# Kernel tuning notes

Hardware: AMD Instinct MI355X
Metric: run time of the kernel (lower is better)

Reference implementation:

```python
import jax, jax.numpy as jnp
import numpy as np

N, E, L, HID, HEADS, G = 50000, 800000, 2, 128, 8, 256
DK = HID // HEADS

def _ln(x, g, b, eps=1e-5):
    m = jnp.mean(x, axis=-1, keepdims=True)
    v = jnp.mean((x - m) ** 2, axis=-1, keepdims=True)
    return (x - m) * jax.lax.rsqrt(v + eps) * g + b

def setup_inputs() -> dict:
    key = jax.random.key(0)
    ks = jax.random.split(key, 24)
    rn = lambda i, s: (0.05 * jax.random.normal(ks[i], s)).astype(jnp.float32)
    return {
        'node_attr': jax.random.randint(ks[0], (N, 4), 0, 64, dtype=jnp.int32),
        'batch_idx': jnp.sort(jax.random.randint(ks[1], (N,), 0, G, dtype=jnp.int32)),
        'edge_index': jax.random.randint(ks[2], (2, E), 0, N, dtype=jnp.int32),
        'strat_dist': jax.random.randint(ks[3], (E,), 0, 32, dtype=jnp.int32),
        'strat_path': jax.random.randint(ks[4], (E,), 0, 16, dtype=jnp.int32),
        'atom_emb': rn(5, (4, 64, HID)),
        'dist_emb': rn(6, (L, 32, HID)),
        'path_emb': rn(7, (L, 16, HID)),
        'Wq': rn(8, (L, HID, HID)), 'bq': rn(9, (L, HID)),
        'Wk': rn(10, (L, HID, HID)), 'bk': rn(11, (L, HID)),
        'Wv': rn(12, (L, HID, HID)), 'bv': rn(13, (L, HID)),
        'Wa': rn(14, (L, HID, HID)), 'ba': rn(15, (L, HID)),
        'ln1_g': jnp.ones((L, HID), jnp.float32), 'ln1_b': jnp.zeros((L, HID), jnp.float32),
        'Wmid': rn(16, (L, HID, 2 * HID)), 'bmid': rn(17, (L, 2 * HID)),
        'Wo': rn(18, (L, 2 * HID, HID)), 'bo': rn(19, (L, HID)),
        'ln2_g': jnp.ones((L, HID), jnp.float32), 'ln2_b': jnp.zeros((L, HID), jnp.float32),
        'W_out': rn(20, (HID, 1)), 'b_out': jnp.zeros((1,), jnp.float32),
    }

def reference(node_attr, batch_idx, edge_index, strat_dist, strat_path,
              atom_emb, dist_emb, path_emb, Wq, bq, Wk, bk, Wv, bv, Wa, ba,
              ln1_g, ln1_b, Wmid, bmid, Wo, bo, ln2_g, ln2_b, W_out, b_out):
    # node encoder: sum of per-feature embeddings (AtomEncoder style)
    x = sum(atom_emb[f][node_attr[:, f]] for f in range(node_attr.shape[1]))  # [N, HID]
    src, tgt = edge_index[0], edge_index[1]  # j (source), i (target)
    inv_sqrt_dk = np.float32(1.0 / np.sqrt(DK))
    for l in range(L):
        # per-edge gather + relational encodings added to the source vector
        s = x[src] + dist_emb[l][strat_dist] + path_emb[l][strat_path]  # [E, HID]
        t = x[tgt]                                                      # [E, HID]
        q = (t @ Wq[l] + bq[l]).reshape(E, HEADS, DK)
        k = (s @ Wk[l] + bk[l]).reshape(E, HEADS, DK)
        v = (s @ Wv[l] + bv[l]).reshape(E, HEADS, DK)
        scores = jnp.sum(q * k, axis=-1) * inv_sqrt_dk  # [E, HEADS]
        # segment softmax keyed on target node id
        smax = jax.ops.segment_max(scores, tgt, num_segments=N)
        ex = jnp.exp(scores - smax[tgt])
        den = jax.ops.segment_sum(ex, tgt, num_segments=N)
        att = ex / (den[tgt] + 1e-16)                   # [E, HEADS]
        msg = (v * att[:, :, None]).reshape(E, HID)
        aggr = jax.ops.segment_sum(msg, tgt, num_segments=N)  # scatter-add
        # update: attn FFN + residual + LayerNorms (dropout is identity in eval)
        h = _ln(jax.nn.gelu(aggr, approximate=False) @ Wa[l] + ba[l] + x, ln1_g[l], ln1_b[l])
        h2 = jax.nn.gelu(h @ Wmid[l] + bmid[l], approximate=False) @ Wo[l] + bo[l]
        x = _ln(h2 + h, ln2_g[l], ln2_b[l])
    # global mean pool per graph, then readout
    cnt = jax.ops.segment_sum(jnp.ones((N,), x.dtype), batch_idx, num_segments=G)
    pooled = jax.ops.segment_sum(x, batch_idx, num_segments=G) / jnp.maximum(cnt, 1.0)[:, None]
    return pooled @ W_out + b_out
```

## Files before the change

### kernel.cpp

```cpp
#include <hip/hip_runtime.h>
#include <hip/hip_bf16.h>
#include <math.h>
#include <stdint.h>

#define N_NODES 50000
#define N_EDGES 800000
#define HID 128
#define NGRAPH 256
#define NLAYER 2
#define CAP 64

#define SCATH 704
#define EHALF 360448
#define SCATQ 859

#define CPAD 5

#define ENC_B 3125
#define TKV_B (ENC_B + 1024)
#define RPK_B (TKV_B + 128)
#define PREP_B (RPK_B + 4)

typedef __bf16 bf16x8 __attribute__((ext_vector_type(8)));
typedef __bf16 bf16x2 __attribute__((ext_vector_type(2)));
typedef float f32x4 __attribute__((ext_vector_type(4)));
typedef float f32x2 __attribute__((ext_vector_type(2)));

__device__ __forceinline__ float gelu_f(float v) {
    return 0.5f * v * (1.0f + erff(v * 0.70710678118654752f));
}

__device__ __forceinline__ f32x2 f8lo(uint32_t d) {
    return __builtin_amdgcn_cvt_pk_f32_fp8((int)d, false);
}
__device__ __forceinline__ f32x2 f8hi(uint32_t d) {
    return __builtin_amdgcn_cvt_pk_f32_fp8((int)d, true);
}
__device__ __forceinline__ uint32_t pk4_fp8(float a, float b, float c, float d) {
    int w = __builtin_amdgcn_cvt_pk_fp8_f32(a, b, 0, false);
    w = __builtin_amdgcn_cvt_pk_fp8_f32(c, d, w, true);
    return (uint32_t)w;
}
__device__ __forceinline__ f32x2 bfpair(uint32_t d) {
    f32x2 r;
    r[0] = __uint_as_float(d << 16);
    r[1] = __uint_as_float(d);
    return r;
}

__device__ __forceinline__ void scatter_block(
    int blk, int ebase, int elim,
    const int* __restrict__ tgt, const int* __restrict__ src,
    const int* __restrict__ sd, const int* __restrict__ sp,
    int* __restrict__ cnt, uint32_t* __restrict__ ei) {
    int tid = threadIdx.x;
    int e0 = ebase + blk * 512 + tid;
    int e1 = e0 + 256;
    bool v0 = e0 < elim;
    bool v1 = e1 < elim;
    int t0 = 0, t1 = 0;
    uint32_t p0 = 0, p1 = 0;
    if (v0) {
        t0 = tgt[e0];
        p0 = (uint32_t)src[e0] | ((uint32_t)((sd[e0] << 4) | sp[e0]) << 16);
    }
    if (v1) {
        t1 = tgt[e1];
        p1 = (uint32_t)src[e1] | ((uint32_t)((sd[e1] << 4) | sp[e1]) << 16);
    }
    int r0 = CAP, r1 = CAP;
    if (v0) r0 = atomicAdd(&cnt[t0 << CPAD], 1);
    if (v1) r1 = atomicAdd(&cnt[t1 << CPAD], 1);
    if (v0 && r0 < CAP) ei[(t0 << 6) + r0] = p0;
    if (v1 && r1 < CAP) ei[(t1 << 6) + r1] = p1;
}

__global__ __launch_bounds__(256) void prep_kernel(
    const int* __restrict__ attr, const float* __restrict__ aemb,
    __bf16* __restrict__ xb,
    const float* __restrict__ de, const float* __restrict__ pe,
    const float* __restrict__ Wk, const float* __restrict__ Wv,
    __bf16* __restrict__ tkv,
    const float* __restrict__ Wq, const float* __restrict__ Wa,
    const float* __restrict__ Wmid, const float* __restrict__ Wo,
    __bf16* __restrict__ wqkvf, __bf16* __restrict__ waf,
    __bf16* __restrict__ wmidf, __bf16* __restrict__ wof,
    const int* __restrict__ batch, const float* __restrict__ bout,
    const float* __restrict__ bq, const float* __restrict__ bk,
    const float* __restrict__ bv,
    float* __restrict__ invc, float* __restrict__ outp, float* __restrict__ bqkv,
    const int* __restrict__ tgt, const int* __restrict__ src,
    const int* __restrict__ sd, const int* __restrict__ sp,
    int* __restrict__ cnt, uint32_t* __restrict__ ei) {
    __shared__ float sde[128];
    int b = blockIdx.x;
    int tid = threadIdx.x;
    if (b < SCATH) {
        scatter_block(b, 0, EHALF, tgt, src, sd, sp, cnt, ei);
        return;
    }
    b -= SCATH;
    if (b < ENC_B) {
        int gid = b * 256 + tid;
        int n = gid >> 4;
        int c8 = (gid & 15) << 3;
        const int4 a = *(const int4*)(attr + n * 4);
        const float* r0 = aemb + (size_t)(0 * 64 + a.x) * 128 + c8;
        const float* r1 = aemb + (size_t)(1 * 64 + a.y) * 128 + c8;
        const float* r2 = aemb + (size_t)(2 * 64 + a.z) * 128 + c8;
        const float* r3 = aemb + (size_t)(3 * 64 + a.w) * 128 + c8;
        f32x4 v0a = *(const f32x4*)r0, v0b = *(const f32x4*)(r0 + 4);
        f32x4 v1a = *(const f32x4*)r1, v1b = *(const f32x4*)(r1 + 4);
        f32x4 v2a = *(const f32x4*)r2, v2b = *(const f32x4*)(r2 + 4);
        f32x4 v3a = *(const f32x4*)r3, v3b = *(const f32x4*)(r3 + 4);
        bf16x8 o;
#pragma unroll
        for (int j = 0; j < 4; j++) {
            o[j] = (__bf16)(v0a[j] + v1a[j] + v2a[j] + v3a[j]);
            o[4 + j] = (__bf16)(v0b[j] + v1b[j] + v2b[j] + v3b[j]);
        }
        *(bf16x8*)(xb + (size_t)n * 128 + c8) = o;
    } else if (b < TKV_B) {
        int bb = b - ENC_B;
        int l = bb >> 9;
        int md = bb & 511;
        int dd = md >> 4, pp = md & 15;
        int c = tid;
        if (c < 128) sde[c] = de[l * 4096 + dd * 128 + c] + pe[l * 2048 + pp * 128 + c];
        __syncthreads();
        const float* W = (c < 128) ? (Wk + l * 16384) : (Wv + l * 16384);
        int cc = c & 127;
        float acc = 0.f;
#pragma unroll 4
        for (int k = 0; k < 128; k++) acc = fmaf(sde[k], W[k * 128 + cc], acc);
        tkv[(size_t)bb * 256 + c] = (__bf16)acc;
    } else if (b < RPK_B) {
        int u = (b - TKV_B) * 256 + tid;
        int l = u >> 14, r = u & 16383;
        const float* srcp;
        __bf16* dstp;
        int kg, scol, srcCO;
        if (r < 6144) {
            kg = r / 384;
            int uu = r % 384;
            int sec = uu >> 7, cc = uu & 127;
            scol = ((cc & 15) << 3) | (cc >> 4);
            const float* Ws = (sec == 0) ? Wq : (sec == 1) ? Wk : Wv;
            srcp = Ws + l * 16384;
            srcCO = 128;
            dstp = wqkvf + (size_t)l * 49152 + (size_t)r * 8;
        } else if (r < 8192) {
            int rr = r - 6144;
            kg = rr >> 7;
            int cc = rr & 127;
            scol = ((cc & 15) << 3) | (cc >> 4);
            srcp = Wa + l * 16384;
            srcCO = 128;
            dstp = waf + (size_t)l * 16384 + (size_t)rr * 8;
        } else if (r < 12288) {
            int rr = r - 8192;
            kg = rr >> 8;
            int uu = rr & 255;
            int blk = uu >> 7, cc = uu & 127;
            scol = blk * 128 + (((cc & 15) << 3) | (cc >> 4));
            srcp = Wmid + l * 32768;
            srcCO = 256;
            dstp = wmidf + (size_t)l * 32768 + (size_t)rr * 8;
        } else {
            int rr = r - 12288;
            kg = rr >> 7;
            int cc = rr & 127;
            scol = ((cc & 15) << 3) | (cc >> 4);
            srcp = Wo + l * 32768;
            srcCO = 128;
            dstp = wof + (size_t)l * 32768 + (size_t)rr * 8;
        }
        bf16x8 o;
#pragma unroll
        for (int j = 0; j < 8; j++) o[j] = (__bf16)srcp[(kg * 8 + j) * srcCO + scol];
        *(bf16x8*)dstp = o;
    } else {
        int sb = b - RPK_B;
        if (sb == 0) {
            int g = tid;
            int lo = 0, hi = N_NODES;
            while (lo < hi) { int mid = (lo + hi) >> 1; if (batch[mid] < g) lo = mid + 1; else hi = mid; }
            int start = lo;
            lo = start; hi = N_NODES;
            while (lo < hi) { int mid = (lo + hi) >> 1; if (batch[mid] < g + 1) lo = mid + 1; else hi = mid; }
            int c2 = lo - start;
            invc[g] = 1.0f / fmaxf((float)c2, 1.0f);
            outp[g] = bout[0];
        } else {
            int r = (sb - 1) * 256 + tid;
            int l = r / 384, c = r % 384;
            float v = (c < 128) ? bq[l * 128 + c]
                    : (c < 256) ? bk[l * 128 + c - 128]
                                : bv[l * 128 + c - 256];
            bqkv[r] = v;
        }
    }
}

__global__ __launch_bounds__(256) void qkv_gemm(
    const __bf16* __restrict__ A, const __bf16* __restrict__ Wf,
    const float* __restrict__ bias, __bf16* __restrict__ Qb,
    uint8_t* __restrict__ kv8, int M, int scatN,
    const int* __restrict__ tgt, const int* __restrict__ src,
    const int* __restrict__ sd, const int* __restrict__ sp,
    int* __restrict__ cnt, uint32_t* __restrict__ ei) {
    int tid = threadIdx.x;
    if (blockIdx.x < (unsigned)scatN) {
        scatter_block(blockIdx.x, EHALF, N_EDGES, tgt, src, sd, sp, cnt, ei);
        return;
    }
    int bq = blockIdx.x - scatN;
    int sec = bq % 3;
    int rowblk = bq / 3;
    int lane = tid & 63;
    int wv = tid >> 6;
    int row0 = rowblk * 64 + wv * 16;
    int col0 = sec * 128;
    if (row0 >= M) return;
    int quad = lane >> 4, tq = lane & 15;
    f32x4 acc[8] = {};
#pragma unroll
    for (int k0 = 0; k0 < 128; k0 += 32) {
        int rr = row0 + tq;
        if (rr >= M) rr = M - 1;
        bf16x8 af = *(const bf16x8*)(A + (size_t)rr * 128 + k0 + quad * 8);
#pragma unroll
        for (int nt = 0; nt < 8; nt++) {
            bf16x8 bfr = *(const bf16x8*)(Wf + ((size_t)((k0 >> 3) + quad) * 384 + col0 + nt * 16 + tq) * 8);
            acc[nt] = __builtin_amdgcn_mfma_f32_16x16x32_bf16(af, bfr, acc[nt], 0, 0, 0);
        }
    }
    int cb = tq * 8;
    float bia[8];
#pragma unroll
    for (int t = 0; t < 8; t++) bia[t] = bias[col0 + cb + t];
#pragma unroll
    for (int v = 0; v < 4; v++) {
        int rr = row0 + quad * 4 + v;
        if (rr >= M) continue;
        float val[8];
#pragma unroll
        for (int t = 0; t < 8; t++) val[t] = acc[t][v] + bia[t];
        if (sec == 0) {
            bf16x8 ov;
#pragma unroll
            for (int t = 0; t < 8; t++) ov[t] = (__bf16)val[t];
            *(bf16x8*)(Qb + (size_t)rr * 128 + cb) = ov;
        } else {
            uint2 st;
            st.x = pk4_fp8(val[0], val[1], val[2], val[3]);
            st.y = pk4_fp8(val[4], val[5], val[6], val[7]);
            *(uint2*)(kv8 + (size_t)rr * 256 + (sec - 1) * 128 + cb) = st;
        }
    }
}

template <bool POOL>
__global__ __launch_bounds__(256) void ffn_uber(
    const __bf16* __restrict__ A,
    const __bf16* __restrict__ xres,
    const __bf16* __restrict__ Waf, const float* __restrict__ ba,
    const float* __restrict__ l1g, const float* __restrict__ l1b,
    const __bf16* __restrict__ Wmf, const float* __restrict__ bmid,
    const __bf16* __restrict__ Wof, const float* __restrict__ bo,
    const float* __restrict__ l2g, const float* __restrict__ l2b,
    __bf16* __restrict__ outx,
    const int* __restrict__ batch, const float* __restrict__ invc,
    const float* __restrict__ WoutV, float* __restrict__ outp,
    int M) {
    __shared__ __bf16 hld[4][16][136];
    __shared__ __bf16 smid[4][16][264];
    __shared__ float ps[POOL ? NGRAPH : 1];
    int lane = threadIdx.x & 63;
    int wv = threadIdx.x >> 6;
    int row0 = blockIdx.x * 64 + wv * 16;
    bool active = row0 < M;
    if (POOL) {
        ps[threadIdx.x] = 0.f;
        __syncthreads();
    } else if (!active) {
        return;
    }
    int quad = lane >> 4, tq = lane & 15;
    if (active) {
        int cb = tq * 8;
        {
            f32x4 acc[8] = {};
#pragma unroll
            for (int k0 = 0; k0 < 128; k0 += 32) {
                int rr = row0 + tq;
                if (rr >= M) rr = M - 1;
                bf16x8 af = *(const bf16x8*)(A + (size_t)rr * 128 + k0 + quad * 8);
#pragma unroll
                for (int nt = 0; nt < 8; nt++) {
                    bf16x8 bfr = *(const bf16x8*)(Waf + ((size_t)((k0 >> 3) + quad) * 128 + nt * 16 + tq) * 8);
                    acc[nt] = __builtin_amdgcn_mfma_f32_16x16x32_bf16(af, bfr, acc[nt], 0, 0, 0);
                }
            }
            float bia[8], gv[8], bv2[8];
#pragma unroll
            for (int t = 0; t < 8; t++) {
                bia[t] = ba[cb + t];
                gv[t] = l1g[cb + t];
                bv2[t] = l1b[cb + t];
            }
#pragma unroll
            for (int v = 0; v < 4; v++) {
                int rr = row0 + quad * 4 + v;
                int rc = (rr < M) ? rr : M - 1;
                bf16x8 rv = *(const bf16x8*)(xres + (size_t)rc * 128 + cb);
                float val[8];
#pragma unroll
                for (int t = 0; t < 8; t++) val[t] = acc[t][v] + bia[t] + (float)rv[t];
                float s = 0.f, s2 = 0.f;
#pragma unroll
                for (int t = 0; t < 8; t++) { s += val[t]; s2 = fmaf(val[t], val[t], s2); }
#pragma unroll
                for (int o = 1; o < 16; o <<= 1) {
                    s += __shfl_xor(s, o);
                    s2 += __shfl_xor(s2, o);
                }
                float m = s * (1.0f / 128.0f);
                float var = s2 * (1.0f / 128.0f) - m * m;
                float rs = rsqrtf(var + 1e-5f);
                bf16x8 ov;
#pragma unroll
                for (int t = 0; t < 8; t++) ov[t] = (__bf16)((val[t] - m) * rs * gv[t] + bv2[t]);
                *(bf16x8*)(&hld[wv][quad * 4 + v][cb]) = ov;
            }
        }
        asm volatile("" ::: "memory");
#pragma unroll
        for (int cH = 0; cH < 2; ++cH) {
            f32x4 acc[8] = {};
#pragma unroll
            for (int k0 = 0; k0 < 128; k0 += 32) {
                bf16x8 af = *(const bf16x8*)(&hld[wv][tq][k0 + quad * 8]);
#pragma unroll
                for (int nt = 0; nt < 8; nt++) {
                    bf16x8 bfr = *(const bf16x8*)(Wmf + ((size_t)((k0 >> 3) + quad) * 256 + cH * 128 + nt * 16 + tq) * 8);
                    acc[nt] = __builtin_amdgcn_mfma_f32_16x16x32_bf16(af, bfr, acc[nt], 0, 0, 0);
                }
            }
            int cb2 = cH * 128 + cb;
            float bia[8];
#pragma unroll
            for (int t = 0; t < 8; t++) bia[t] = bmid[cb2 + t];
#pragma unroll
            for (int v = 0; v < 4; v++) {
                bf16x8 ov;
#pragma unroll
                for (int t = 0; t < 8; t++) ov[t] = (__bf16)gelu_f(acc[t][v] + bia[t]);
                *(bf16x8*)(&smid[wv][quad * 4 + v][cb2]) = ov;
            }
        }
        asm volatile("" ::: "memory");
        f32x4 acc[8] = {};
#pragma unroll
        for (int k0 = 0; k0 < 256; k0 += 32) {
            bf16x8 af = *(const bf16x8*)(&smid[wv][tq][k0 + quad * 8]);
#pragma unroll
            for (int nt = 0; nt < 8; nt++) {
                bf16x8 bfr = *(const bf16x8*)(Wof + ((size_t)((k0 >> 3) + quad) * 128 + nt * 16 + tq) * 8);
                acc[nt] = __builtin_amdgcn_mfma_f32_16x16x32_bf16(af, bfr, acc[nt], 0, 0, 0);
            }
        }
        float bia[8], gv[8], bv2[8], wo8[8];
#pragma unroll
        for (int t = 0; t < 8; t++) {
            bia[t] = bo[cb + t];
            gv[t] = l2g[cb + t];
            bv2[t] = l2b[cb + t];
        }
        if (POOL) {
#pragma unroll
            for (int t = 0; t < 8; t++) wo8[t] = WoutV[cb + t];
        }
#pragma unroll
        for (int v = 0; v < 4; v++) {
            int rr = row0 + quad * 4 + v;
            bf16x8 rv = *(const bf16x8*)(&hld[wv][quad * 4 + v][cb]);
            float val[8];
#pragma unroll
            for (int t = 0; t < 8; t++) val[t] = acc[t][v] + bia[t] + (float)rv[t];
            float s = 0.f, s2 = 0.f;
#pragma unroll
            for (int t = 0; t < 8; t++) { s += val[t]; s2 = fmaf(val[t], val[t], s2); }
#pragma unroll
            for (int o = 1; o < 16; o <<= 1) {
                s += __shfl_xor(s, o);
                s2 += __shfl_xor(s2, o);
            }
            float m = s * (1.0f / 128.0f);
            float var = s2 * (1.0f / 128.0f) - m * m;
            float rs = rsqrtf(var + 1e-5f);
#pragma unroll
            for (int t = 0; t < 8; t++) val[t] = (val[t] - m) * rs * gv[t] + bv2[t];
            if (rr >= M) continue;
            if (!POOL) {
                bf16x8 ov;
#pragma unroll
                for (int t = 0; t < 8; t++) ov[t] = (__bf16)val[t];
                *(bf16x8*)(outx + (size_t)rr * 128 + cb) = ov;
            } else {
                float dot = 0.f;
#pragma unroll
                for (int t = 0; t < 8; t++) dot = fmaf(val[t], wo8[t], dot);
#pragma unroll
                for (int o = 1; o < 16; o <<= 1) dot += __shfl_xor(dot, o);
                if (tq == 0) {
                    int g = batch[rr];
                    atomicAdd(&ps[g], dot * invc[g]);
                }
            }
        }
    }
    if (POOL) {
        __syncthreads();
        float pv = ps[threadIdx.x];
        if (pv != 0.f) atomicAdd(&outp[threadIdx.x], pv);
    }
}

__global__ __launch_bounds__(256) void attn_kernel(
    const __bf16* __restrict__ Qb, const uint8_t* __restrict__ kv8,
    const __bf16* __restrict__ tkv,
    const int* __restrict__ cnt, const uint32_t* __restrict__ ei,
    __bf16* __restrict__ outb) {
    __shared__ float red[4][1376];
    int wv = threadIdx.x >> 6;
    int i = blockIdx.x * 4 + wv;
    int lane = threadIdx.x & 63;
    int slot = lane >> 3, h = lane & 7;
    int ch0 = h * 16;
    const uint4* qv = (const uint4*)(Qb + (size_t)i * 128 + ch0);
    uint4 qa = qv[0], qb = qv[1];
    uint32_t qd[8] = {qa.x, qa.y, qa.z, qa.w, qb.x, qb.y, qb.z, qb.w};
    f32x2 qp[8];
#pragma unroll
    for (int j = 0; j < 8; j++) qp[j] = bfpair(qd[j]);
    int deg = cnt[i << CPAD];
    if (deg > CAP) deg = CAP;
    int p0 = i << 6;
    int p1 = p0 + deg;
    float l = 0.f;
    f32x2 ap[8] = {};
    int p = p0 + slot;
    uint32_t w1 = 0, w2 = 0;
    if (p < p1) w1 = ei[p];
    if (p + 8 < p1) w2 = ei[p + 8];
    uint4 kw, vw, t0, t1, u0, u1;
    {
        int j = w1 & 0xffff, md = w1 >> 16;
        const uint8_t* kr = kv8 + (size_t)j * 256 + ch0;
        kw = *(const uint4*)kr;
        vw = *(const uint4*)(kr + 128);
        const __bf16* tr = tkv + md * 256 + ch0;
        t0 = *(const uint4*)tr;
        t1 = *(const uint4*)(tr + 8);
        u0 = *(const uint4*)(tr + 128);
        u1 = *(const uint4*)(tr + 136);
    }
    while (p < p1) {
        uint4 kwn, vwn, t0n, t1n, u0n, u1n;
        {
            int j = w2 & 0xffff, md = w2 >> 16;
            const uint8_t* kr = kv8 + (size_t)j * 256 + ch0;
            kwn = *(const uint4*)kr;
            vwn = *(const uint4*)(kr + 128);
            const __bf16* tr = tkv + md * 256 + ch0;
            t0n = *(const uint4*)tr;
            t1n = *(const uint4*)(tr + 8);
            u0n = *(const uint4*)(tr + 128);
            u1n = *(const uint4*)(tr + 136);
        }
        int pn = p + 16;
        uint32_t w3 = ei[(pn < p1) ? pn : p];
        uint32_t kd[4] = {kw.x, kw.y, kw.z, kw.w};
        uint32_t vd[4] = {vw.x, vw.y, vw.z, vw.w};
        uint32_t td[8] = {t0.x, t0.y, t0.z, t0.w, t1.x, t1.y, t1.z, t1.w};
        uint32_t ud[8] = {u0.x, u0.y, u0.z, u0.w, u1.x, u1.y, u1.z, u1.w};
        f32x2 sa = {0.f, 0.f};
#pragma unroll
        for (int j = 0; j < 4; j++) {
            f32x2 klo = f8lo(kd[j]) + bfpair(td[2 * j]);
            f32x2 khi = f8hi(kd[j]) + bfpair(td[2 * j + 1]);
            sa = qp[2 * j] * klo + sa;
            sa = qp[2 * j + 1] * khi + sa;
        }
        float s = sa[0] + sa[1];
        float pe = __expf(s * 0.25f);
        l += pe;
        f32x2 pp = {pe, pe};
#pragma unroll
        for (int j = 0; j < 4; j++) {
            f32x2 vlo = f8lo(vd[j]) + bfpair(ud[2 * j]);
            f32x2 vhi = f8hi(vd[j]) + bfpair(ud[2 * j + 1]);
            ap[2 * j] = pp * vlo + ap[2 * j];
            ap[2 * j + 1] = pp * vhi + ap[2 * j + 1];
        }
        kw = kwn; vw = vwn; t0 = t0n; t1 = t1n; u0 = u0n; u1 = u1n;
        w2 = w3;
        p += 8;
    }
    float* rw = red[wv] + slot * 172 + 20 * h;
#pragma unroll
    for (int j = 0; j < 8; j++) *(f32x2*)(rw + 2 * j) = ap[j];
    red[wv][slot * 172 + 156 + h] = l;
    asm volatile("" ::: "memory");
    int pc = 2 * lane + 4 * (lane >> 3);
    int hh = lane >> 3;
    float s0 = 0.f, s1 = 0.f, ls = 0.f;
#pragma unroll
    for (int s = 0; s < 8; s++) {
        float2 v = *(const float2*)(red[wv] + s * 172 + pc);
        s0 += v.x;
        s1 += v.y;
        ls += red[wv][s * 172 + 156 + hh];
    }
    float inv = 1.0f / (ls + 1e-16f);
    bf16x2 o2;
    o2[0] = (__bf16)gelu_f(s0 * inv);
    o2[1] = (__bf16)gelu_f(s1 * inv);
    *(bf16x2*)(outb + (size_t)i * 128 + 2 * lane) = o2;
}

extern "C" void kernel_launch(void* const* d_in, const int* in_sizes, int n_in,
                              void* d_out, int out_size, void* d_ws, size_t ws_size,
                              hipStream_t stream) {
    const int N = N_NODES, E = N_EDGES;
    const int* node_attr = (const int*)d_in[0];
    const int* batch_idx = (const int*)d_in[1];
    const int* edge_index = (const int*)d_in[2];
    const int* strat_dist = (const int*)d_in[3];
    const int* strat_path = (const int*)d_in[4];
    const float* atom_emb = (const float*)d_in[5];
    const float* dist_emb = (const float*)d_in[6];
    const float* path_emb = (const float*)d_in[7];
    const float* Wq = (const float*)d_in[8];
    const float* bq = (const float*)d_in[9];
    const float* Wk = (const float*)d_in[10];
    const float* bk = (const float*)d_in[11];
    const float* Wv = (const float*)d_in[12];
    const float* bv = (const float*)d_in[13];
    const float* Wa = (const float*)d_in[14];
    const float* ba = (const float*)d_in[15];
    const float* ln1g = (const float*)d_in[16];
    const float* ln1b = (const float*)d_in[17];
    const float* Wmid = (const float*)d_in[18];
    const float* bmid = (const float*)d_in[19];
    const float* Wo = (const float*)d_in[20];
    const float* bo = (const float*)d_in[21];
    const float* ln2g = (const float*)d_in[22];
    const float* ln2b = (const float*)d_in[23];
    const float* Wout = (const float*)d_in[24];
    const float* bout = (const float*)d_in[25];
    float* out = (float*)d_out;

    const int* src = edge_index;
    const int* tgt = edge_index + E;

    size_t NF = (size_t)N * HID;
    float* invc = (float*)d_ws;
    float* bqkv = invc + 256;
    __bf16* xb = (__bf16*)(bqkv + 768);
    __bf16* Qb = xb + NF;
    __bf16* ab = Qb + NF;
    __bf16* tkv = ab + NF;
    __bf16* wqkvf = tkv + 262144;
    __bf16* waf = wqkvf + 98304;
    __bf16* wmidf = waf + 32768;
    __bf16* wof = wmidf + 65536;
    uint8_t* kv8 = (uint8_t*)(wof + 65536);
    uint32_t* ei = (uint32_t*)(kv8 + (size_t)N * 256);
    int* cnt = (int*)(ei + (size_t)N * CAP);

    hipMemsetAsync(cnt, 0, (size_t)N * 32 * sizeof(int), stream);
    prep_kernel<<<SCATH + PREP_B, 256, 0, stream>>>(
        node_attr, atom_emb, xb,
        dist_emb, path_emb, Wk, Wv, tkv,
        Wq, Wa, Wmid, Wo, wqkvf, waf, wmidf, wof,
        batch_idx, bout, bq, bk, bv, invc, out, bqkv,
        tgt, src, strat_dist, strat_path, cnt, ei);

    const int GB = (N + 63) / 64;
    const int AB = (N + 3) / 4;

    for (int l = 0; l < NLAYER; ++l) {
        int scatN = (l == 0) ? SCATQ : 0;
        qkv_gemm<<<scatN + 3 * GB, 256, 0, stream>>>(
            xb, wqkvf + l * 49152, bqkv + l * 384, Qb, kv8, N, scatN,
            tgt, src, strat_dist, strat_path, cnt, ei);

        attn_kernel<<<AB, 256, 0, stream>>>(Qb, kv8, tkv + l * 131072, cnt, ei, ab);

        if (l < NLAYER - 1) {
            ffn_uber<false><<<GB, 256, 0, stream>>>(
                ab, xb, waf + l * 16384, ba + l * 128, ln1g + l * 128, ln1b + l * 128,
                wmidf + l * 32768, bmid + l * 256, wof + l * 32768, bo + l * 128,
                ln2g + l * 128, ln2b + l * 128, xb,
                nullptr, nullptr, nullptr, nullptr, N);
        } else {
            ffn_uber<true><<<GB, 256, 0, stream>>>(
                ab, xb, waf + l * 16384, ba + l * 128, ln1g + l * 128, ln1b + l * 128,
                wmidf + l * 32768, bmid + l * 256, wof + l * 32768, bo + l * 128,
                ln2g + l * 128, ln2b + l * 128, nullptr,
                batch_idx, invc, Wout, out, N);
        }
    }
}
```

Before: 371.0 us.

## Move all edge bucketing into prep kernel with target-range partitioned scatter

The edge scatter into per-target buckets no longer runs split across the prep kernel and the first QKV GEMM. It now runs entirely in the prep kernel. Each group of 4096 edges is handled by 8 blocks, and each block only inserts edges whose target falls in its 6250-node range, which localizes atomics and bucket writes. The trade-off is that every block reads tgt for all 4096 edges in its group, so target reads are multiplied 8x. The QKV GEMM also loses its overlap with half of the scatter work.

After: 370.1 us. Within noise of the previous version (-0.3%).

```diff
diff --git a/kernel.cpp b/kernel.cpp
--- a/kernel.cpp
+++ b/kernel.cpp
@@ -10,11 +10,11 @@
 #define NLAYER 2
 #define CAP 64
 
-#define SCATH 704
-#define EHALF 360448
-#define SCATQ 859
-
 #define CPAD 5
+
+#define SC_GRP 196
+#define SC_B (SC_GRP * 8)
+#define NPART 6250
 
 #define ENC_B 3125
 #define TKV_B (ENC_B + 1024)
@@ -46,33 +46,6 @@
     r[0] = __uint_as_float(d << 16);
     r[1] = __uint_as_float(d);
     return r;
-}
-
-__device__ __forceinline__ void scatter_block(
-    int blk, int ebase, int elim,
-    const int* __restrict__ tgt, const int* __restrict__ src,
-    const int* __restrict__ sd, const int* __restrict__ sp,
-    int* __restrict__ cnt, uint32_t* __restrict__ ei) {
-    int tid = threadIdx.x;
-    int e0 = ebase + blk * 512 + tid;
-    int e1 = e0 + 256;
-    bool v0 = e0 < elim;
-    bool v1 = e1 < elim;
-    int t0 = 0, t1 = 0;
-    uint32_t p0 = 0, p1 = 0;
-    if (v0) {
-        t0 = tgt[e0];
-        p0 = (uint32_t)src[e0] | ((uint32_t)((sd[e0] << 4) | sp[e0]) << 16);
-    }
-    if (v1) {
-        t1 = tgt[e1];
-        p1 = (uint32_t)src[e1] | ((uint32_t)((sd[e1] << 4) | sp[e1]) << 16);
-    }
-    int r0 = CAP, r1 = CAP;
-    if (v0) r0 = atomicAdd(&cnt[t0 << CPAD], 1);
-    if (v1) r1 = atomicAdd(&cnt[t1 << CPAD], 1);
-    if (v0 && r0 < CAP) ei[(t0 << 6) + r0] = p0;
-    if (v1 && r1 < CAP) ei[(t1 << 6) + r1] = p1;
 }
 
 __global__ __launch_bounds__(256) void prep_kernel(
@@ -95,11 +68,27 @@
     __shared__ float sde[128];
     int b = blockIdx.x;
     int tid = threadIdx.x;
-    if (b < SCATH) {
-        scatter_block(b, 0, EHALF, tgt, src, sd, sp, cnt, ei);
+    if (b < SC_B) {
+        int grp = b >> 3;
+        int part = b & 7;
+        int plo = part * NPART;
+        int phi = plo + NPART;
+        int base = grp * 4096 + tid;
+#pragma unroll
+        for (int k = 0; k < 16; k++) {
+            int e = base + k * 256;
+            if (e < N_EDGES) {
+                int t = tgt[e];
+                if (t >= plo && t < phi) {
+                    uint32_t pk = (uint32_t)src[e] | ((uint32_t)((sd[e] << 4) | sp[e]) << 16);
+                    int r = atomicAdd(&cnt[t << CPAD], 1);
+                    if (r < CAP) ei[(t << 6) + r] = pk;
+                }
+            }
+        }
         return;
     }
-    b -= SCATH;
+    b -= SC_B;
     if (b < ENC_B) {
         int gid = b * 256 + tid;
         int n = gid >> 4;
@@ -205,16 +194,9 @@
 __global__ __launch_bounds__(256) void qkv_gemm(
     const __bf16* __restrict__ A, const __bf16* __restrict__ Wf,
     const float* __restrict__ bias, __bf16* __restrict__ Qb,
-    uint8_t* __restrict__ kv8, int M, int scatN,
-    const int* __restrict__ tgt, const int* __restrict__ src,
-    const int* __restrict__ sd, const int* __restrict__ sp,
-    int* __restrict__ cnt, uint32_t* __restrict__ ei) {
+    uint8_t* __restrict__ kv8, int M) {
     int tid = threadIdx.x;
-    if (blockIdx.x < (unsigned)scatN) {
-        scatter_block(blockIdx.x, EHALF, N_EDGES, tgt, src, sd, sp, cnt, ei);
-        return;
-    }
-    int bq = blockIdx.x - scatN;
+    int bq = blockIdx.x;
     int sec = bq % 3;
     int rowblk = bq / 3;
     int lane = tid & 63;
@@ -581,7 +563,7 @@
     int* cnt = (int*)(ei + (size_t)N * CAP);
 
     hipMemsetAsync(cnt, 0, (size_t)N * 32 * sizeof(int), stream);
-    prep_kernel<<<SCATH + PREP_B, 256, 0, stream>>>(
+    prep_kernel<<<SC_B + PREP_B, 256, 0, stream>>>(
         node_attr, atom_emb, xb,
         dist_emb, path_emb, Wk, Wv, tkv,
         Wq, Wa, Wmid, Wo, wqkvf, waf, wmidf, wof,
@@ -592,10 +574,8 @@
     const int AB = (N + 3) / 4;
 
     for (int l = 0; l < NLAYER; ++l) {
-        int scatN = (l == 0) ? SCATQ : 0;
-        qkv_gemm<<<scatN + 3 * GB, 256, 0, stream>>>(
-            xb, wqkvf + l * 49152, bqkv + l * 384, Qb, kv8, N, scatN,
-            tgt, src, strat_dist, strat_path, cnt, ei);
+        qkv_gemm<<<3 * GB, 256, 0, stream>>>(
+            xb, wqkvf + l * 49152, bqkv + l * 384, Qb, kv8, N);
 
         attn_kernel<<<AB, 256, 0, stream>>>(Qb, kv8, tkv + l * 131072, cnt, ei, ab);
 
```
